# Kernel tuning notes

Hardware: AMD Instinct MI355X
Metric: run time of the kernel (lower is better)

The kernel has to match this reference:

```python
import jax, jax.numpy as jnp
import numpy as np

B, N, F, E, H, A, V, L = 128, 196, 512, 512, 512, 512, 30000, 21


def setup_inputs() -> dict:
    key = jax.random.key(0)
    ks = jax.random.split(key, 20)
    s = 0.02
    d = {
        "feats": jax.random.normal(ks[0], (B, N, F), jnp.float32),
        "captions": jax.random.randint(ks[1], (B, L), 1, V),
        "embed_W": (jax.random.normal(ks[2], (V, E), jnp.float32) * s).at[0].set(0.0),
        "Wf_w": jax.random.normal(ks[3], (A, F), jnp.float32) * s,
        "Wf_b": jnp.zeros((A,), jnp.float32),
        "Wh_w": jax.random.normal(ks[4], (A, H), jnp.float32) * s,
        "Wh_b": jnp.zeros((A,), jnp.float32),
        "v_w": jax.random.normal(ks[5], (1, A), jnp.float32) * s,
        "v_b": jnp.zeros((1,), jnp.float32),
        "W_ih": jax.random.normal(ks[6], (4 * H, E + F), jnp.float32) * s,
        "W_hh": jax.random.normal(ks[7], (4 * H, H), jnp.float32) * s,
        "b_ih": jnp.zeros((4 * H,), jnp.float32),
        "b_hh": jnp.zeros((4 * H,), jnp.float32),
        "init_w": jax.random.normal(ks[8], (H, F), jnp.float32) * s,
        "init_b": jnp.zeros((H,), jnp.float32),
        "initc_w": jax.random.normal(ks[9], (H, F), jnp.float32) * s,
        "initc_b": jnp.zeros((H,), jnp.float32),
        "out_w": jax.random.normal(ks[10], (V, H), jnp.float32) * s,
        "out_b": jnp.zeros((V,), jnp.float32),
    }
    return d


def reference(feats, captions, embed_W, Wf_w, Wf_b, Wh_w, Wh_b, v_w, v_b,
              W_ih, W_hh, b_ih, b_hh, init_w, init_b, initc_w, initc_b,
              out_w, out_b):
    # padding_idx=0 -> embedding row 0 is zero
    emW = embed_W.at[0].set(0.0)
    emb = emW[captions[:, :-1]]                       # [B, T, E], T = L-1
    gfeat = feats.mean(axis=1)                        # [B, F]
    h0 = gfeat @ init_w.T + init_b                    # [B, H]
    c0 = gfeat @ initc_w.T + initc_b                  # [B, H]
    # attention feature projection is timestep-invariant: hoist out of loop
    fproj = jnp.einsum('bnf,af->bna', feats, Wf_w) + Wf_b  # [B, N, A]

    def step(carry, emb_t):
        h, c = carry
        hproj = h @ Wh_w.T + Wh_b                     # [B, A]
        e = jnp.tanh(fproj + hproj[:, None, :])       # [B, N, A]
        scores = jnp.einsum('bna,a->bn', e, v_w[0]) + v_b[0]
        w = jax.nn.softmax(scores, axis=1)            # [B, N]
        ctx = jnp.einsum('bnf,bn->bf', feats, w)      # [B, F]
        x = jnp.concatenate([emb_t, ctx], axis=1)     # [B, E+F]
        gates = x @ W_ih.T + b_ih + h @ W_hh.T + b_hh # [B, 4H]
        i, f, g, o = jnp.split(gates, 4, axis=1)      # torch gate order i,f,g,o
        i = jax.nn.sigmoid(i)
        f = jax.nn.sigmoid(f)
        g = jnp.tanh(g)
        o = jax.nn.sigmoid(o)
        c = f * c + i * g
        h = o * jnp.tanh(c)
        logit = h @ out_w.T + out_b                   # [B, V]
        return (h, c), logit

    _, logits = jax.lax.scan(step, (h0, c0), jnp.swapaxes(emb, 0, 1))
    return jnp.swapaxes(logits, 0, 1)                 # [B, T, V]
```

## Files before the change

### kernel.cpp

```cpp
#include <hip/hip_runtime.h>
#include <stdint.h>
#include <stddef.h>

typedef unsigned short u16;
typedef __attribute__((ext_vector_type(8))) short short8;
typedef __attribute__((ext_vector_type(4))) float f32x4;

#define DEV static __device__ __forceinline__

DEV float bf2f(u16 u){ return __uint_as_float(((unsigned)u)<<16); }
DEV u16 f2bf(float f){ unsigned x=__float_as_uint(f); return (u16)((x + 0x7fffu + ((x>>16)&1u))>>16); }

DEV float wsum(float v){
#pragma unroll
  for(int o=32;o;o>>=1) v += __shfl_xor(v,o);
  return v;
}
DEV float wmax(float v){
#pragma unroll
  for(int o=32;o;o>>=1) v = fmaxf(v,__shfl_xor(v,o));
  return v;
}
DEV float sigm(float x){ return __fdividef(1.f, 1.f+__expf(-x)); }
DEV float tanhx(float x){ float e=__expf(-2.f*fabsf(x)); float t=__fdividef(1.f-e,1.f+e); return x<0.f?-t:t; }

DEV f32x4 mfma16(short8 a, short8 b, f32x4 c){
  asm("v_mfma_f32_16x16x32_bf16 %0, %1, %2, %0" : "+v"(c) : "v"(a), "v"(b));
  return c;
}
DEV void gll16(const void* g, void* l){
  __builtin_amdgcn_global_load_lds((const __attribute__((address_space(1))) void*)g,
                                   (__attribute__((address_space(3))) void*)l, 16, 0, 0);
}

DEV void pack8(u16* dst, const float* src){
  const float4 a=*(const float4*)(src);
  const float4 b=*(const float4*)(src+4);
  short8 o;
  o[0]=(short)f2bf(a.x); o[1]=(short)f2bf(a.y); o[2]=(short)f2bf(a.z); o[3]=(short)f2bf(a.w);
  o[4]=(short)f2bf(b.x); o[5]=(short)f2bf(b.y); o[6]=(short)f2bf(b.z); o[7]=(short)f2bf(b.w);
  *(short8*)dst=o;
}
DEV void zero8(u16* dst){
  short8 z;
#pragma unroll
  for(int e=0;e<8;++e) z[e]=0;
  *(short8*)dst=z;
}

__global__ __launch_bounds__(256) void setup_cast(
  const float* __restrict__ feats, const int* __restrict__ captions,
  const float* __restrict__ embW, const float* __restrict__ Wf_w,
  const float* __restrict__ Wh_w, const float* __restrict__ W_ih,
  const float* __restrict__ W_hh, const float* __restrict__ b_ih,
  const float* __restrict__ b_hh, const float* __restrict__ out_w,
  u16* __restrict__ feats_bf, u16* __restrict__ outw_bf, u16* __restrict__ Wc,
  u16* __restrict__ WihE, u16* __restrict__ embx, u16* __restrict__ Whw_bf,
  u16* __restrict__ Wf_bf, float* __restrict__ bias_comb)
{
  const long long o0=12845056LL,o1=28246016LL,o2=30343168LL,o3=31391744LL,
                  o4=32702464LL,o5=32964608LL,o6=33226752LL,total=33228800LL;
  for (long long i8=((long long)blockIdx.x*256+threadIdx.x)*8; i8<total;
       i8+=(long long)gridDim.x*256*8){
    const long long i=i8;
    if (i<o0){ pack8(feats_bf+i, feats+i); }
    else if (i<o1){ const long long j=i-o0; const int r=(int)(j>>9);
      if (r<30000) pack8(outw_bf+j, out_w+j); else zero8(outw_bf+j); }
    else if (i<o2){ const long long j=i-o1; const int r=(int)(j>>10), k=(int)(j&1023);
      const int o=((r&3)<<9)+(r>>2);
      const float* s=(k<512)? (W_ih+(size_t)o*1024+512+k) : (W_hh+(size_t)o*512+(k-512));
      pack8(Wc+j, s); }
    else if (i<o3){ const long long j=i-o2; const int r=(int)(j>>9), k=(int)(j&511);
      const int o=((r&3)<<9)+(r>>2);
      pack8(WihE+j, W_ih+(size_t)o*1024+k); }
    else if (i<o4){ const long long j=i-o3; const int m=(int)(j>>9), e=(int)(j&511);
      const int b=m/20, tt=m-b*20; const int idx=captions[b*21+tt];
      if (idx) pack8(embx+j, embW+(size_t)idx*512+e); else zero8(embx+j); }
    else if (i<o5){ const long long j=i-o4; pack8(Whw_bf+j, Wh_w+j); }
    else if (i<o6){ const long long j=i-o5; pack8(Wf_bf+j, Wf_w+j); }
    else { const long long j=i-o6;
      for(int e=0;e<8;++e){ const int r=(int)(j+e); const int o=((r&3)<<9)+(r>>2);
        bias_comb[r]=b_ih[o]+b_hh[o]; } }
  }
}

__global__ __launch_bounds__(256) void prep(
  const float* __restrict__ feats, const float* __restrict__ init_w,
  const float* __restrict__ init_b, const float* __restrict__ initc_w,
  const float* __restrict__ initc_b, u16* __restrict__ xs0, float* __restrict__ cbuf)
{
  const int b=blockIdx.x, tid=threadIdx.x, lane=tid&63, w=tid>>6;
  __shared__ float gf[512];
  const float* fb=feats+(size_t)b*196*512;
  float a0=0.f,a1=0.f;
  for(int n=0;n<196;++n){ a0+=fb[(size_t)n*512+tid]; a1+=fb[(size_t)n*512+tid+256]; }
  gf[tid]=a0*(1.f/196.f); gf[tid+256]=a1*(1.f/196.f);
  __syncthreads();
  const int kb=lane*8;
  float g8[8];
#pragma unroll
  for(int e=0;e<8;++e) g8[e]=gf[kb+e];
  for(int j=w*128;j<w*128+128;++j){
    const float* r1=init_w+(size_t)j*512+kb;
    const float* r2=initc_w+(size_t)j*512+kb;
    float s1=0.f,s2=0.f;
#pragma unroll
    for(int e=0;e<8;++e){ s1+=g8[e]*r1[e]; s2+=g8[e]*r2[e]; }
    s1=wsum(s1); s2=wsum(s2);
    if(lane==(j&63)){ xs0[b*1024+512+j]=f2bf(s1+init_b[j]); cbuf[b*512+j]=s2+initc_b[j]; }
  }
}

__global__ __launch_bounds__(1024) void attn_step(
  const u16* __restrict__ fproj, const u16* __restrict__ feats_bf,
  u16* __restrict__ xs, const u16* __restrict__ Whw,
  const float* __restrict__ Whb, const float* __restrict__ vw,
  const float* __restrict__ vb, const float* __restrict__ gemb,
  const float* __restrict__ gpart, float* __restrict__ cbuf,
  u16* __restrict__ h_all, int t)
{
  const int b=blockIdx.x, tid=threadIdx.x, lane=tid&63, w=tid>>6;
  __shared__ float part[16][512];
  __shared__ float hsf[512], hp[512], sc[208], red[16];
  if (t>0){
    if (tid<512){
      const int u=tid;
      float4 g4=*(const float4*)&gemb[((size_t)b*20+(t-1))*2048+u*4];
#pragma unroll
      for(int kz=0;kz<8;++kz){
        const float4 p=*(const float4*)&gpart[((size_t)kz*128+b)*2048+u*4];
        g4.x+=p.x; g4.y+=p.y; g4.z+=p.z; g4.w+=p.w;
      }
      const float cn=sigm(g4.y)*cbuf[b*512+u]+sigm(g4.x)*tanhx(g4.z);
      const float hn=sigm(g4.w)*tanhx(cn);
      cbuf[b*512+u]=cn;
      const u16 hb=f2bf(hn);
      xs[b*1024+512+u]=hb;
      h_all[((size_t)b*20+(t-1))*512+u]=hb;
      hsf[u]=bf2f(hb);
    }
  } else {
    if (tid<512) hsf[tid]=bf2f(xs[b*1024+512+tid]);
  }
  __syncthreads();
  const int kb=lane*8;
  float h8[8];
#pragma unroll
  for(int e=0;e<8;++e) h8[e]=hsf[kb+e];
#pragma unroll
  for(int jj=0;jj<32;jj+=8){
    const int j=w*32+jj;
    short8 wv[8];
#pragma unroll
    for(int r=0;r<8;++r) wv[r]=*(const short8*)(Whw+(size_t)(j+r)*512+kb);
    float s[8];
#pragma unroll
    for(int r=0;r<8;++r) s[r]=0.f;
#pragma unroll
    for(int e=0;e<8;++e){
      const float he=h8[e];
#pragma unroll
      for(int r=0;r<8;++r) s[r]+=he*bf2f((u16)wv[r][e]);
    }
#pragma unroll
    for(int r=0;r<8;++r) s[r]=wsum(s[r]);
    if(lane==0){
#pragma unroll
      for(int r=0;r<8;++r) hp[j+r]=s[r]+Whb[j+r];
    }
  }
  __syncthreads();
  float p2[8], vm2[8];
  float sv=0.f;
#pragma unroll
  for(int e=0;e<8;++e){
    const float p=hp[kb+e], v=vw[kb+e];
    p2[e]=2.f*p; vm2[e]=-2.f*v; sv+=v;
  }
  const float vb0=vb[0];
#pragma unroll
  for(int i=0;i<12;i+=6){
    const int n0=w+16*i;
    short8 f[6];
#pragma unroll
    for(int r=0;r<6;++r) f[r]=*(const short8*)(fproj+((size_t)b*196+n0+16*r)*512+kb);
    float s[6];
#pragma unroll
    for(int r=0;r<6;++r) s[r]=sv;
#pragma unroll
    for(int e=0;e<8;++e){
#pragma unroll
      for(int r=0;r<6;++r)
        s[r]+=__fdividef(vm2[e],__expf(fmaf(bf2f((u16)f[r][e]),2.f,p2[e]))+1.f);
    }
#pragma unroll
    for(int r=0;r<6;++r) s[r]=wsum(s[r]);
    if(lane==0){
#pragma unroll
      for(int r=0;r<6;++r) sc[n0+16*r]=s[r]+vb0;
    }
  }
  {
    const int n=w+192;
    if (n<196){
      short8 f0=*(const short8*)(fproj+((size_t)b*196+n)*512+kb);
      float s0=sv;
#pragma unroll
      for(int e=0;e<8;++e)
        s0+=__fdividef(vm2[e],__expf(fmaf(bf2f((u16)f0[e]),2.f,p2[e]))+1.f);
      s0=wsum(s0);
      if(lane==0) sc[n]=s0+vb0;
    }
  }
  __syncthreads();
  float xv=(tid<196)? sc[tid] : -3.0e38f;
  float mx=wmax(xv);
  if(lane==0) red[w]=mx;
  __syncthreads();
  float mm=red[0];
#pragma unroll
  for(int i=1;i<16;++i) mm=fmaxf(mm,red[i]);
  float pv=(tid<196)? __expf(xv-mm) : 0.f;
  float ps=wsum(pv);
  __syncthreads();
  if(lane==0) red[w]=ps;
  __syncthreads();
  float tot=red[0];
#pragma unroll
  for(int i=1;i<16;++i) tot+=red[i];
  if(tid<196) sc[tid]=__fdividef(pv,tot);
  __syncthreads();
  float a8[8];
#pragma unroll
  for(int e=0;e<8;++e) a8[e]=0.f;
#pragma unroll
  for(int i=0;i<12;i+=6){
    const int n0=w+16*i;
    short8 v[6];
#pragma unroll
    for(int r=0;r<6;++r) v[r]=*(const short8*)(feats_bf+((size_t)b*196+n0+16*r)*512+kb);
    float wn[6];
#pragma unroll
    for(int r=0;r<6;++r) wn[r]=sc[n0+16*r];
#pragma unroll
    for(int e=0;e<8;++e){
      float acc=a8[e];
#pragma unroll
      for(int r=0;r<6;++r) acc+=wn[r]*bf2f((u16)v[r][e]);
      a8[e]=acc;
    }
  }
  {
    const int n=w+192;
    if (n<196){
      short8 v0=*(const short8*)(feats_bf+((size_t)b*196+n)*512+kb);
      const float wn=sc[n];
#pragma unroll
      for(int e=0;e<8;++e) a8[e]+=wn*bf2f((u16)v0[e]);
    }
  }
  *(float4*)&part[w][kb]  =*(float4*)&a8[0];
  *(float4*)&part[w][kb+4]=*(float4*)&a8[4];
  __syncthreads();
  if (tid<512){
    float s=0.f;
#pragma unroll
    for(int i=0;i<16;++i) s+=part[i][tid];
    xs[b*1024+tid]=f2bf(s);
  }
}

__global__ __launch_bounds__(512) void lstm_fin(
  const float* __restrict__ gemb, const float* __restrict__ gpart,
  const float* __restrict__ cbuf, u16* __restrict__ h_all)
{
  const int b=blockIdx.x, u=threadIdx.x;
  float4 g4=*(const float4*)&gemb[((size_t)b*20+19)*2048+u*4];
#pragma unroll
  for(int kz=0;kz<8;++kz){
    const float4 p=*(const float4*)&gpart[((size_t)kz*128+b)*2048+u*4];
    g4.x+=p.x; g4.y+=p.y; g4.z+=p.z; g4.w+=p.w;
  }
  const float cn=sigm(g4.y)*cbuf[b*512+u]+sigm(g4.x)*tanhx(g4.z);
  const float hn=sigm(g4.w)*tanhx(cn);
  h_all[((size_t)b*20+19)*512+u]=f2bf(hn);
}

template<int MODE>
__global__ __launch_bounds__(256) void gemm_bt(
  const u16* __restrict__ A, int lda, const u16* __restrict__ Bw, int ldb, int K,
  const float* __restrict__ bias, float* __restrict__ outf, u16* __restrict__ outb,
  int ncols)
{
  const int bm=(MODE==4)? 0 : ((MODE==2)? blockIdx.x*128 : blockIdx.y*128);
  const int bn=(MODE==2)? blockIdx.y*128 : blockIdx.x*128;
  const int kz=(MODE==4)? blockIdx.y : 0;
  const u16* __restrict__ Ap=A +(size_t)kz*K;
  const u16* __restrict__ Bp=Bw+(size_t)kz*K;
  const int tid=threadIdx.x, lane=tid&63, wave=tid>>6;
  const int wr=(wave>>1)*64, wc=(wave&1)*64;
  __shared__ u16 As[128*32], Bs[128*32];
  f32x4 acc[4][4]={};
  const int srow=tid>>2, scol=(tid&3)*8;
  for(int k0=0;k0<K;k0+=32){
    gll16(Ap+(size_t)(bm+srow)*lda    +k0+scol, As+tid*8);
    gll16(Ap+(size_t)(bm+64+srow)*lda +k0+scol, As+2048+tid*8);
    gll16(Bp+(size_t)(bn+srow)*ldb    +k0+scol, Bs+tid*8);
    gll16(Bp+(size_t)(bn+64+srow)*ldb +k0+scol, Bs+2048+tid*8);
    __syncthreads();
    short8 af[4], bfr[4];
    const int ro=lane&15, ko=(lane>>4)*8;
#pragma unroll
    for(int m=0;m<4;++m) af[m]=*(const short8*)(As+(wr+m*16+ro)*32+ko);
#pragma unroll
    for(int n=0;n<4;++n) bfr[n]=*(const short8*)(Bs+(wc+n*16+ro)*32+ko);
#pragma unroll
    for(int m=0;m<4;++m)
#pragma unroll
      for(int n=0;n<4;++n) acc[m][n]=mfma16(af[m],bfr[n],acc[m][n]);
    __syncthreads();
  }
  asm volatile("s_nop 7\ns_nop 7\ns_nop 7");
  const int ro4=(lane>>4)*4, co=lane&15;
#pragma unroll
  for(int m=0;m<4;++m)
#pragma unroll
    for(int n=0;n<4;++n)
#pragma unroll
      for(int j=0;j<4;++j){
        const int r=bm+wr+m*16+ro4+j, c=bn+wc+n*16+co;
        if constexpr (MODE==0)      outb[(size_t)r*ncols+c]=f2bf(acc[m][n][j]+bias[c]);
        else if constexpr (MODE==1) outf[(size_t)r*ncols+c]=acc[m][n][j]+bias[c];
        else if constexpr (MODE==2){ if (c<ncols) outf[(size_t)r*ncols+c]=acc[m][n][j]+bias[c]; }
        else                        outf[((size_t)kz*128+r)*ncols+c]=acc[m][n][j];
      }
}

extern "C" void kernel_launch(void* const* d_in, const int* in_sizes, int n_in,
                              void* d_out, int out_size, void* d_ws, size_t ws_size,
                              hipStream_t stream) {
  const float* feats   =(const float*)d_in[0];
  const int*   captions=(const int*)  d_in[1];
  const float* embW    =(const float*)d_in[2];
  const float* Wf_w    =(const float*)d_in[3];
  const float* Wf_b    =(const float*)d_in[4];
  const float* Wh_w    =(const float*)d_in[5];
  const float* Wh_b    =(const float*)d_in[6];
  const float* v_w     =(const float*)d_in[7];
  const float* v_b     =(const float*)d_in[8];
  const float* W_ih    =(const float*)d_in[9];
  const float* W_hh    =(const float*)d_in[10];
  const float* b_ih    =(const float*)d_in[11];
  const float* b_hh    =(const float*)d_in[12];
  const float* init_w  =(const float*)d_in[13];
  const float* init_b  =(const float*)d_in[14];
  const float* initc_w =(const float*)d_in[15];
  const float* initc_b =(const float*)d_in[16];
  const float* out_w   =(const float*)d_in[17];
  const float* out_b   =(const float*)d_in[18];
  float* out=(float*)d_out;
  char* ws=(char*)d_ws;

  u16*   feats_bf =(u16*)  (ws+0);
  u16*   fproj    =(u16*)  (ws+25690112);
  u16*   outw_bf  =(u16*)  (ws+51380224);
  u16*   Wc       =(u16*)  (ws+82182144);
  u16*   WihE     =(u16*)  (ws+86376448);
  u16*   Whw_bf   =(u16*)  (ws+88473600);
  u16*   Wf_bf    =(u16*)  (ws+88997888);
  u16*   embx     =(u16*)  (ws+89522176);
  u16*   h_all    =(u16*)  (ws+92143616);
  u16*   xs0      =(u16*)  (ws+94765056);
  float* gemb     =(float*)(ws+95289344);
  float* cbuf     =(float*)(ws+116260864);
  float* bias_comb=(float*)(ws+116785152);
  float* gpart    =(float*)(ws+116793344);

  setup_cast<<<4096,256,0,stream>>>(feats,captions,embW,Wf_w,Wh_w,W_ih,W_hh,b_ih,b_hh,out_w,
                                    feats_bf,outw_bf,Wc,WihE,embx,Whw_bf,Wf_bf,bias_comb);
  prep<<<128,256,0,stream>>>(feats,init_w,init_b,initc_w,initc_b,xs0,cbuf);
  gemm_bt<0><<<dim3(4,196),256,0,stream>>>(feats_bf,512,Wf_bf,512,512,
      Wf_b,nullptr,fproj,512);
  gemm_bt<1><<<dim3(16,20),256,0,stream>>>(embx,512,WihE,512,512,
      bias_comb,gemb,nullptr,2048);

  for(int t=0;t<20;++t){
    attn_step<<<128,1024,0,stream>>>(fproj,feats_bf,xs0,Whw_bf,Wh_b,v_w,v_b,
                                     gemb,gpart,cbuf,h_all,t);
    gemm_bt<4><<<dim3(16,8),256,0,stream>>>(xs0,1024,Wc,1024,128,
        nullptr,gpart,nullptr,2048);
  }
  lstm_fin<<<128,512,0,stream>>>(gemb,gpart,cbuf,h_all);
  gemm_bt<2><<<dim3(20,235),256,0,stream>>>(h_all,512,outw_bf,512,512,
      out_b,out,nullptr,30000);
}
```

Baseline: 1.141 ms.

## Split per-batch attention step across two cooperating blocks with flag sync

Each batch row's attention step now runs on a pair of 1024-thread blocks instead of one. Each block computes half of the 196 attention scores and writes them to global memory, then waits on the partner through an acquire/release flag spin. Both blocks redo the softmax, and each produces half of the context vector. The cell state is double-buffered by timestep parity so the two blocks do not race on it. This doubles the parallelism across 256 CUs, at the cost of a global round-trip and spin-wait that depends on both blocks of a pair being resident at the same time.

```diff
diff --git a/kernel.cpp b/kernel.cpp
--- a/kernel.cpp
+++ b/kernel.cpp
@@ -4,6 +4,7 @@
 
 typedef unsigned short u16;
 typedef __attribute__((ext_vector_type(8))) short short8;
+typedef __attribute__((ext_vector_type(4))) short short4v;
 typedef __attribute__((ext_vector_type(4))) float f32x4;
 
 #define DEV static __device__ __forceinline__
@@ -111,17 +112,19 @@
   }
 }
 
-__global__ __launch_bounds__(1024) void attn_step(
+__global__ __launch_bounds__(1024) void attn_pair(
   const u16* __restrict__ fproj, const u16* __restrict__ feats_bf,
   u16* __restrict__ xs, const u16* __restrict__ Whw,
   const float* __restrict__ Whb, const float* __restrict__ vw,
   const float* __restrict__ vb, const float* __restrict__ gemb,
   const float* __restrict__ gpart, float* __restrict__ cbuf,
-  u16* __restrict__ h_all, int t)
+  u16* __restrict__ h_all, float* __restrict__ sc_g,
+  unsigned* __restrict__ flags, int t)
 {
-  const int b=blockIdx.x, tid=threadIdx.x, lane=tid&63, w=tid>>6;
-  __shared__ float part[16][512];
-  __shared__ float hsf[512], hp[512], sc[208], red[16];
+  const int blk=blockIdx.x, tid=threadIdx.x, lane=tid&63, w=tid>>6;
+  const int b=blk>>1, h=blk&1;
+  __shared__ float part[16][256];
+  __shared__ float hsf[512], hp[512], scw[208], red[16];
   if (t>0){
     if (tid<512){
       const int u=tid;
@@ -131,9 +134,10 @@
         const float4 p=*(const float4*)&gpart[((size_t)kz*128+b)*2048+u*4];
         g4.x+=p.x; g4.y+=p.y; g4.z+=p.z; g4.w+=p.w;
       }
-      const float cn=sigm(g4.y)*cbuf[b*512+u]+sigm(g4.x)*tanhx(g4.z);
+      const float cold=cbuf[((t-1)&1)*65536 + b*512+u];
+      const float cn=sigm(g4.y)*cold+sigm(g4.x)*tanhx(g4.z);
       const float hn=sigm(g4.w)*tanhx(cn);
-      cbuf[b*512+u]=cn;
+      cbuf[(t&1)*65536 + b*512+u]=cn;
       const u16 hb=f2bf(hn);
       xs[b*1024+512+u]=hb;
       h_all[((size_t)b*20+(t-1))*512+u]=hb;
@@ -178,9 +182,8 @@
     p2[e]=2.f*p; vm2[e]=-2.f*v; sv+=v;
   }
   const float vb0=vb[0];
-#pragma unroll
-  for(int i=0;i<12;i+=6){
-    const int n0=w+16*i;
+  {
+    const int n0=98*h+w;
     short8 f[6];
 #pragma unroll
     for(int r=0;r<6;++r) f[r]=*(const short8*)(fproj+((size_t)b*196+n0+16*r)*512+kb);
@@ -197,76 +200,76 @@
     for(int r=0;r<6;++r) s[r]=wsum(s[r]);
     if(lane==0){
 #pragma unroll
-      for(int r=0;r<6;++r) sc[n0+16*r]=s[r]+vb0;
-    }
+      for(int r=0;r<6;++r) sc_g[b*224+n0+16*r]=s[r]+vb0;
+    }
+  }
+  if (w<2){
+    const int n=98*h+96+w;
+    short8 f0=*(const short8*)(fproj+((size_t)b*196+n)*512+kb);
+    float s0=sv;
+#pragma unroll
+    for(int e=0;e<8;++e)
+      s0+=__fdividef(vm2[e],__expf(fmaf(bf2f((u16)f0[e]),2.f,p2[e]))+1.f);
+    s0=wsum(s0);
+    if(lane==0) sc_g[b*224+n]=s0+vb0;
+  }
+  __syncthreads();
+  if (tid==0){
+    __threadfence();
+    __hip_atomic_store(&flags[blk],(unsigned)(t+1),__ATOMIC_RELEASE,__HIP_MEMORY_SCOPE_AGENT);
+    while(__hip_atomic_load(&flags[blk^1],__ATOMIC_ACQUIRE,__HIP_MEMORY_SCOPE_AGENT)<(unsigned)(t+1))
+      __builtin_amdgcn_s_sleep(1);
+    __threadfence();
+  }
+  __syncthreads();
+  float xv=(tid<196)? sc_g[b*224+tid] : -3.0e38f;
+  float mx=wmax(xv);
+  if(lane==0) red[w]=mx;
+  __syncthreads();
+  float mm=red[0];
+#pragma unroll
+  for(int i=1;i<16;++i) mm=fmaxf(mm,red[i]);
+  float pv=(tid<196)? __expf(xv-mm) : 0.f;
+  float ps=wsum(pv);
+  __syncthreads();
+  if(lane==0) red[w]=ps;
+  __syncthreads();
+  float tot=red[0];
+#pragma unroll
+  for(int i=1;i<16;++i) tot+=red[i];
+  if(tid<196) scw[tid]=__fdividef(pv,tot);
+  __syncthreads();
+  float4 acc; acc.x=0.f; acc.y=0.f; acc.z=0.f; acc.w=0.f;
+  const int cb=h*256+lane*4;
+#pragma unroll
+  for(int i=0;i<12;i+=2){
+    const int n0=w+16*i, n1=n0+16;
+    short4v v0=*(const short4v*)(feats_bf+((size_t)b*196+n0)*512+cb);
+    short4v v1=*(const short4v*)(feats_bf+((size_t)b*196+n1)*512+cb);
+    const float w0=scw[n0], w1=scw[n1];
+    acc.x+=w0*bf2f((u16)v0[0])+w1*bf2f((u16)v1[0]);
+    acc.y+=w0*bf2f((u16)v0[1])+w1*bf2f((u16)v1[1]);
+    acc.z+=w0*bf2f((u16)v0[2])+w1*bf2f((u16)v1[2]);
+    acc.w+=w0*bf2f((u16)v0[3])+w1*bf2f((u16)v1[3]);
   }
   {
     const int n=w+192;
     if (n<196){
-      short8 f0=*(const short8*)(fproj+((size_t)b*196+n)*512+kb);
-      float s0=sv;
-#pragma unroll
-      for(int e=0;e<8;++e)
-        s0+=__fdividef(vm2[e],__expf(fmaf(bf2f((u16)f0[e]),2.f,p2[e]))+1.f);
-      s0=wsum(s0);
-      if(lane==0) sc[n]=s0+vb0;
-    }
-  }
-  __syncthreads();
-  float xv=(tid<196)? sc[tid] : -3.0e38f;
-  float mx=wmax(xv);
-  if(lane==0) red[w]=mx;
-  __syncthreads();
-  float mm=red[0];
-#pragma unroll
-  for(int i=1;i<16;++i) mm=fmaxf(mm,red[i]);
-  float pv=(tid<196)? __expf(xv-mm) : 0.f;
-  float ps=wsum(pv);
-  __syncthreads();
-  if(lane==0) red[w]=ps;
-  __syncthreads();
-  float tot=red[0];
-#pragma unroll
-  for(int i=1;i<16;++i) tot+=red[i];
-  if(tid<196) sc[tid]=__fdividef(pv,tot);
-  __syncthreads();
-  float a8[8];
-#pragma unroll
-  for(int e=0;e<8;++e) a8[e]=0.f;
-#pragma unroll
-  for(int i=0;i<12;i+=6){
-    const int n0=w+16*i;
-    short8 v[6];
-#pragma unroll
-    for(int r=0;r<6;++r) v[r]=*(const short8*)(feats_bf+((size_t)b*196+n0+16*r)*512+kb);
-    float wn[6];
-#pragma unroll
-    for(int r=0;r<6;++r) wn[r]=sc[n0+16*r];
-#pragma unroll
-    for(int e=0;e<8;++e){
-      float acc=a8[e];
-#pragma unroll
-      for(int r=0;r<6;++r) acc+=wn[r]*bf2f((u16)v[r][e]);
-      a8[e]=acc;
-    }
-  }
-  {
-    const int n=w+192;
-    if (n<196){
-      short8 v0=*(const short8*)(feats_bf+((size_t)b*196+n)*512+kb);
-      const float wn=sc[n];
-#pragma unroll
-      for(int e=0;e<8;++e) a8[e]+=wn*bf2f((u16)v0[e]);
-    }
-  }
-  *(float4*)&part[w][kb]  =*(float4*)&a8[0];
-  *(float4*)&part[w][kb+4]=*(float4*)&a8[4];
-  __syncthreads();
-  if (tid<512){
+      short4v v0=*(const short4v*)(feats_bf+((size_t)b*196+n)*512+cb);
+      const float w0=scw[n];
+      acc.x+=w0*bf2f((u16)v0[0]);
+      acc.y+=w0*bf2f((u16)v0[1]);
+      acc.z+=w0*bf2f((u16)v0[2]);
+      acc.w+=w0*bf2f((u16)v0[3]);
+    }
+  }
+  *(float4*)&part[w][lane*4]=acc;
+  __syncthreads();
+  if (tid<256){
     float s=0.f;
 #pragma unroll
     for(int i=0;i<16;++i) s+=part[i][tid];
-    xs[b*1024+tid]=f2bf(s);
+    xs[b*1024 + h*256 + tid]=f2bf(s);
   }
 }
 
@@ -281,7 +284,7 @@
     const float4 p=*(const float4*)&gpart[((size_t)kz*128+b)*2048+u*4];
     g4.x+=p.x; g4.y+=p.y; g4.z+=p.z; g4.w+=p.w;
   }
-  const float cn=sigm(g4.y)*cbuf[b*512+u]+sigm(g4.x)*tanhx(g4.z);
+  const float cn=sigm(g4.y)*cbuf[65536 + b*512+u]+sigm(g4.x)*tanhx(g4.z);
   const float hn=sigm(g4.w)*tanhx(cn);
   h_all[((size_t)b*20+19)*512+u]=f2bf(hn);
 }
@@ -375,7 +378,10 @@
   float* cbuf     =(float*)(ws+116260864);
   float* bias_comb=(float*)(ws+116785152);
   float* gpart    =(float*)(ws+116793344);
-
+  float* sc_g     =(float*)(ws+125200000);
+  unsigned* flags =(unsigned*)(ws+125400064);
+
+  hipMemsetAsync(flags, 0, 1024, stream);
   setup_cast<<<4096,256,0,stream>>>(feats,captions,embW,Wf_w,Wh_w,W_ih,W_hh,b_ih,b_hh,out_w,
                                     feats_bf,outw_bf,Wc,WihE,embx,Whw_bf,Wf_bf,bias_comb);
   prep<<<128,256,0,stream>>>(feats,init_w,init_b,initc_w,initc_b,xs0,cbuf);
@@ -385,8 +391,8 @@
       bias_comb,gemb,nullptr,2048);
 
   for(int t=0;t<20;++t){
-    attn_step<<<128,1024,0,stream>>>(fproj,feats_bf,xs0,Whw_bf,Wh_b,v_w,v_b,
-                                     gemb,gpart,cbuf,h_all,t);
+    attn_pair<<<256,1024,0,stream>>>(fproj,feats_bf,xs0,Whw_bf,Wh_b,v_w,v_b,
+                                     gemb,gpart,cbuf,h_all,sc_g,flags,t);
     gemm_bt<4><<<dim3(16,8),256,0,stream>>>(xs0,1024,Wc,1024,128,
         nullptr,gpart,nullptr,2048);
   }
```

New measurement: 1.329 ms. +16.5%, slower.
